# Optimization experiments

Hardware: AMD Instinct MI355X
Metric: run time of the kernel (lower is better)

## Reference

```python
import jax, jax.numpy as jnp
import numpy as np

B, S, HID = 2, 4096, 2048
H, D = 16, 128
BS = 64            # block_size
SR = 0.5           # sparsity_ratio
NB = S // BS       # number of diagonal blocks
SCALE = D ** -0.5


def setup_inputs() -> dict:
    key = jax.random.key(0)
    ks = jax.random.split(key, 7)
    s = 0.02
    return {
        "hidden_states": jax.random.normal(ks[0], (B, S, HID), jnp.float32),
        "Wq": jax.random.normal(ks[1], (HID, H * D), jnp.float32) * s,
        "Wk": jax.random.normal(ks[2], (HID, H * D), jnp.float32) * s,
        "Wv": jax.random.normal(ks[3], (HID, H * D), jnp.float32) * s,
        "Wo": jax.random.normal(ks[4], (H * D, HID), jnp.float32) * s,
        "Wr": jax.random.normal(ks[5], (HID, H), jnp.float32) * s,   # block_router weight
        "br": jax.random.normal(ks[6], (H,), jnp.float32) * s,       # block_router bias
    }


def reference(hidden_states, Wq, Wk, Wv, Wo, Wr, br):
    # projections: torch Linear(x) == x @ W^T; weights stored pre-transposed here
    q = (hidden_states @ Wq).reshape(B, S, H, D).transpose(0, 2, 1, 3)  # [B,H,S,D]
    k = (hidden_states @ Wk).reshape(B, S, H, D).transpose(0, 2, 1, 3)
    v = (hidden_states @ Wv).reshape(B, S, H, D).transpose(0, 2, 1, 3)

    # per-head routing score, mean-pooled over batch (as in torch: routing_scores[:, h].mean())
    routing = jax.nn.sigmoid(hidden_states.mean(axis=1) @ Wr + br)      # [B,H]
    head_score = routing.mean(axis=0)                                   # [H]
    eff_sparsity = SR * (1.0 - head_score * 0.5)
    # torch: max(1, int(block_size * eff)); positive -> floor == int truncation
    attend_count = jnp.maximum(1, jnp.floor(BS * eff_sparsity).astype(jnp.int32))  # [H]

    # block-diagonal attention: only within-block scores are ever finite, so we
    # never materialize the full SxS matrix (softmax over -inf elsewhere is a no-op)
    qb = q.reshape(B, H, NB, BS, D)
    kb = k.reshape(B, H, NB, BS, D)
    vb = v.reshape(B, H, NB, BS, D)
    scores = jnp.einsum("bhnqd,bhnkd->bhnqk", qb, kb) * SCALE           # [B,H,NB,BS,BS]

    # rank of each key within its row (descending); keep == variable-k top-k mask.
    order = jnp.argsort(-scores, axis=-1)
    rank = jnp.argsort(order, axis=-1)
    keep = rank < attend_count[None, :, None, None, None]
    # non-top-k in-block entries are scattered as 0.0 (not -inf) in the original
    masked = jnp.where(keep, scores, 0.0)

    probs = jax.nn.softmax(masked.astype(jnp.float32), axis=-1).astype(q.dtype)
    out_b = jnp.einsum("bhnqk,bhnkd->bhnqd", probs, vb)                 # [B,H,NB,BS,D]
    out = out_b.reshape(B, H, S, D).transpose(0, 2, 1, 3).reshape(B, S, H * D)
    return out @ Wo
```

## Files before the change

kernel.cpp:

```cpp
#include <hip/hip_runtime.h>
#include <hip/hip_bf16.h>
#include <cstdint>
#include <cstddef>

#define B_   2
#define S_   4096
#define HIDN 2048
#define H_   16
#define D_   128
#define NB_  64
#define MTOT 8192
#define QKVN 6144
#define SCALE_ 0.08838834764831845f

typedef unsigned short ushort_t;
typedef __attribute__((ext_vector_type(8))) short short8;
typedef __attribute__((ext_vector_type(8))) ushort_t ushort8;
typedef __attribute__((ext_vector_type(4))) float f32x4;

__device__ inline float b2f(ushort_t x){ union{unsigned u; float f;} v; v.u=((unsigned)x)<<16; return v.f; }
__device__ inline ushort_t f2b(float f){ union{unsigned u; float f;} v; v.f=f; unsigned r=(v.u + 0x7FFF + ((v.u>>16)&1))>>16; return (ushort_t)r; }

#define MFMA_BF16(a,b,c) __builtin_amdgcn_mfma_f32_16x16x32_bf16((a),(b),(c),0,0,0)

__device__ inline void async16(const ushort_t* g, ushort_t* l){
  __builtin_amdgcn_global_load_lds(
      (const __attribute__((address_space(1))) void*)g,
      (__attribute__((address_space(3))) void*)l, 16, 0, 0);
}

__global__ void bsa_convpart(const float* __restrict__ hs, ushort_t* __restrict__ hsB,
                             float* __restrict__ part){
  int t = threadIdx.x;
  int c  = blockIdx.x*512 + t*2;
  int sc = blockIdx.y;
  int b  = blockIdx.z;
  const float* p = hs  + ((size_t)b*S_ + (size_t)sc*128)*HIDN + c;
  ushort_t*    q = hsB + ((size_t)b*S_ + (size_t)sc*128)*HIDN + c;
  float s0=0.f, s1=0.f;
  #pragma unroll 8
  for (int i=0;i<128;i++){
    float2 v = *(const float2*)(p + (size_t)i*HIDN);
    s0 += v.x; s1 += v.y;
    unsigned pk = (unsigned)f2b(v.x) | ((unsigned)f2b(v.y)<<16);
    *(unsigned*)(q + (size_t)i*HIDN) = pk;
  }
  part[((b*32+sc)*HIDN)+c]   = s0;
  part[((b*32+sc)*HIDN)+c+1] = s1;
}

__global__ void bsa_router(const float* __restrict__ part, const float* __restrict__ Wr,
                           const float* __restrict__ br, int* __restrict__ counts){
  __shared__ float cm[2*HIDN];
  __shared__ float sig[2*H_];
  int t = threadIdx.x;
  for (int i=t; i<2*HIDN; i+=256){
    int b = i>>11, c = i&(HIDN-1);
    float s=0.f;
    for (int j=0;j<32;j++) s += part[((b*32+j)*HIDN)+c];
    cm[b*HIDN+c] = s * (1.0f/S_);
  }
  __syncthreads();
  {
    int g = t>>3;
    int sl = t&7;
    int b = g>>4, h = g&15;
    float acc = 0.f;
    for (int c=sl; c<HIDN; c+=8) acc += cm[b*HIDN+c]*Wr[c*H_+h];
    acc += __shfl_xor(acc, 4);
    acc += __shfl_xor(acc, 2);
    acc += __shfl_xor(acc, 1);
    if (sl==0) sig[g] = 1.f/(1.f+expf(-(acc + br[h])));
  }
  __syncthreads();
  if (t < H_){
    float score = 0.5f*(sig[t] + sig[H_+t]);
    float eff = 0.5f*(1.0f - score*0.5f);
    int ac = (int)floorf(64.f*eff);
    if (ac < 1) ac = 1;
    counts[t] = ac;
  }
}

__global__ void bsa_transpose(const float* w0, const float* w1, const float* w2, const float* w3,
                              ushort_t* o0, ushort_t* o1, ushort_t* o2, ushort_t* o3){
  const float* src; ushort_t* dst;
  switch(blockIdx.z){
    case 0: src=w0; dst=o0; break;
    case 1: src=w1; dst=o1; break;
    case 2: src=w2; dst=o2; break;
    default: src=w3; dst=o3; break;
  }
  __shared__ ushort_t tile[64*72];
  int t = threadIdx.x;
  int r0 = blockIdx.y*64, c0 = blockIdx.x*64;
  for (int it=0; it<16; it++){
    int f = it*256 + t;
    int r = f>>6, c = f&63;
    tile[r*72+c] = f2b(src[(size_t)(r0+r)*HIDN + (c0+c)]);
  }
  __syncthreads();
  for (int it=0; it<16; it++){
    int f = it*256 + t;
    int cc = f>>6, rr = f&63;
    dst[(size_t)(c0+cc)*HIDN + (r0+rr)] = tile[rr*72+cc];
  }
}

template<int F32OUT, int MINW>
__global__ __launch_bounds__(256, MINW) void bsa_gemm_bt(const ushort_t* __restrict__ A,
                                                   const ushort_t* __restrict__ BT,
                                                   void* __restrict__ Cv,
                                                   int M, int N, int K){
  __shared__ __align__(16) ushort_t As[128*32];
  __shared__ __align__(16) ushort_t Bs[128*32];
  int t = threadIdx.x;
  int w = t>>6, lane = t&63;
  int wr = w>>1, wc = w&1;
  int quad = lane>>4, l16 = lane&15;
  int m0 = blockIdx.y*128, n0 = blockIdx.x*128;

  f32x4 acc[4][4] = {};

  int srow = (w*2)*16 + (lane>>2);
  int scol = (lane&3)*8;

  for (int k0=0; k0<K; k0+=32){
    #pragma unroll
    for (int i=0;i<2;i++){
      int chunk = w*2+i;
      const ushort_t* ga = A  + (size_t)(m0 + srow + i*16)*K + k0 + scol;
      const ushort_t* gb = BT + (size_t)(n0 + srow + i*16)*K + k0 + scol;
      async16(ga, &As[chunk*512]);
      async16(gb, &Bs[chunk*512]);
    }
    __syncthreads();
    short8 a[4], b[4];
    #pragma unroll
    for (int i=0;i<4;i++)
      a[i] = *(const short8*)(&As[(wr*64 + i*16 + l16)*32 + quad*8]);
    #pragma unroll
    for (int j=0;j<4;j++)
      b[j] = *(const short8*)(&Bs[(wc*64 + j*16 + l16)*32 + quad*8]);
    #pragma unroll
    for (int i=0;i<4;i++)
      #pragma unroll
      for (int j=0;j<4;j++)
        acc[i][j] = MFMA_BF16(a[i], b[j], acc[i][j]);
    __syncthreads();
  }

  #pragma unroll
  for (int i=0;i<4;i++)
    #pragma unroll
    for (int j=0;j<4;j++){
      int m = m0 + wr*64 + i*16 + quad*4;
      int n = n0 + wc*64 + j*16 + l16;
      #pragma unroll
      for (int r=0;r<4;r++){
        if (F32OUT) ((float*)Cv)[(size_t)(m+r)*N + n] = acc[i][j][r];
        else        ((ushort_t*)Cv)[(size_t)(m+r)*N + n] = f2b(acc[i][j][r]);
      }
    }
}

__global__ __launch_bounds__(256) void bsa_attn(const ushort_t* __restrict__ QKV,
                                                const int* __restrict__ counts,
                                                ushort_t* __restrict__ O){
  __shared__ __align__(16) ushort_t regA[64*136];
  __shared__ __align__(16) ushort_t regB[64*136];
  __shared__ __align__(16) ushort_t Ps[64*72];
  float* Sc = (float*)regA;

  int t = threadIdx.x, w = t>>6, lane = t&63, quad = lane>>4, l16 = lane&15;
  int bid = blockIdx.x;
  int b  = bid>>10;
  int h  = (bid>>6)&15;
  int nb = bid&63;
  size_t qbase = ((size_t)b*S_ + (size_t)nb*64)*QKVN + (size_t)h*D_;
  size_t obase = ((size_t)b*S_ + (size_t)nb*64)*HIDN + (size_t)h*D_;

  int4 vre[4];
  #pragma unroll
  for (int it=0; it<4; it++){
    int f = it*256 + t;
    int r = f>>4, c = (f&15)*8;
    vre[it] = *(const int4*)(QKV + qbase + 4096 + (size_t)r*QKVN + c);
  }

  #pragma unroll
  for (int it=0; it<4; it++){
    int f = it*256 + t;
    int r = f>>4, c = (f&15)*8;
    *(int4*)(&regA[r*136+c]) = *(const int4*)(QKV + qbase +        (size_t)r*QKVN + c);
    *(int4*)(&regB[r*136+c]) = *(const int4*)(QKV + qbase + 2048 + (size_t)r*QKVN + c);
  }
  __syncthreads();

  f32x4 sacc[4] = {};
  #pragma unroll
  for (int ks=0; ks<4; ks++){
    short8 afr = *(const short8*)(&regA[(w*16 + l16)*136 + ks*32 + quad*8]);
    #pragma unroll
    for (int nt=0; nt<4; nt++){
      short8 bfr = *(const short8*)(&regB[(nt*16 + l16)*136 + ks*32 + quad*8]);
      sacc[nt] = MFMA_BF16(afr, bfr, sacc[nt]);
    }
  }
  __syncthreads();

  #pragma unroll
  for (int nt=0; nt<4; nt++)
    #pragma unroll
    for (int r=0;r<4;r++)
      Sc[(w*16 + quad*4 + r)*68 + nt*16 + l16] = sacc[nt][r]*SCALE_;
  #pragma unroll
  for (int it=0; it<4; it++){
    int f = it*256 + t;
    int r = f>>4, c = (f&15)*8;
    *(int4*)(&regB[r*136+c]) = vre[it];
  }

  int cnt = counts[h];
  for (int g=0; g<4; g++){
    float s[4], v[4];
    #pragma unroll
    for (int rr=0; rr<4; rr++){
      s[rr] = Sc[(w*16 + g*4 + rr)*68 + lane];
      v[rr] = s[rr];
    }
    #pragma unroll
    for (int k=2; k<=64; k<<=1){
      #pragma unroll
      for (int m=k>>1; m>=1; m>>=1){
        #pragma unroll
        for (int rr=0; rr<4; rr++){
          float o = __shfl_xor(v[rr], m);
          bool keepMin = (((lane & k)==0) == ((lane & m)==0));
          float lo = fminf(v[rr], o), hi = fmaxf(v[rr], o);
          v[rr] = keepMin ? lo : hi;
        }
      }
    }
    #pragma unroll
    for (int rr=0; rr<4; rr++){
      float T = __shfl(v[rr], 64 - cnt);
      unsigned long long gt = __ballot(s[rr] > T);
      unsigned long long eq = __ballot(s[rr] == T);
      int G = __popcll(gt);
      int eqr = __popcll(eq & ((1ull<<lane)-1ull));
      bool keep = (s[rr] > T) || ((s[rr] == T) && (eqr < cnt - G));
      float m = keep ? s[rr] : 0.0f;
      float mx = fmaxf(__shfl(v[rr], 63), 0.0f);
      float e = __expf(m - mx);
      float sum = e;
      #pragma unroll
      for (int off=32; off; off>>=1) sum += __shfl_xor(sum, off);
      Ps[(w*16 + g*4 + rr)*72 + lane] = f2b(e/sum);
    }
  }
  __syncthreads();

  f32x4 oacc[4][2] = {};
  #pragma unroll
  for (int ks=0; ks<2; ks++){
    short8 bv[2];
    #pragma unroll
    for (int jj=0; jj<2; jj++){
      int n = (w*2+jj)*16 + l16;
      short8 x;
      #pragma unroll
      for (int j=0;j<8;j++){
        int k = ks*32 + quad*8 + j;
        x[j] = (short)regB[k*136 + n];
      }
      bv[jj] = x;
    }
    #pragma unroll
    for (int mt=0; mt<4; mt++){
      short8 aP = *(const short8*)(&Ps[(mt*16 + l16)*72 + ks*32 + quad*8]);
      #pragma unroll
      for (int jj=0; jj<2; jj++)
        oacc[mt][jj] = MFMA_BF16(aP, bv[jj], oacc[mt][jj]);
    }
  }
  #pragma unroll
  for (int mt=0; mt<4; mt++)
    #pragma unroll
    for (int jj=0; jj<2; jj++){
      int row = mt*16 + quad*4;
      int col = (w*2+jj)*16 + l16;
      #pragma unroll
      for (int r=0;r<4;r++)
        O[obase + (size_t)(row+r)*HIDN + col] = f2b(oacc[mt][jj][r]);
    }
}

extern "C" void kernel_launch(void* const* d_in, const int* in_sizes, int n_in,
                              void* d_out, int out_size, void* d_ws, size_t ws_size,
                              hipStream_t stream) {
  const float* hs = (const float*)d_in[0];
  const float* Wq = (const float*)d_in[1];
  const float* Wk = (const float*)d_in[2];
  const float* Wv = (const float*)d_in[3];
  const float* Wo = (const float*)d_in[4];
  const float* Wr = (const float*)d_in[5];
  const float* br = (const float*)d_in[6];
  float* out = (float*)d_out;
  char* ws = (char*)d_ws;

  const size_t MB = 1024u*1024u;
  float*    part   = (float*)(ws + 0);
  int*      counts = (int*)(ws + 512u*1024u);
  ushort_t* hsB    = (ushort_t*)(ws + 1*MB);
  ushort_t* WqT    = (ushort_t*)(ws + 33*MB);
  ushort_t* WkT    = (ushort_t*)(ws + 41*MB);
  ushort_t* WvT    = (ushort_t*)(ws + 49*MB);
  ushort_t* WoT    = (ushort_t*)(ws + 57*MB);
  ushort_t* QKV    = (ushort_t*)(ws + 65*MB);
  ushort_t* AO     = hsB;

  bsa_convpart  <<<dim3(4,32,2),  256, 0, stream>>>(hs, hsB, part);
  bsa_router    <<<1,             256, 0, stream>>>(part, Wr, br, counts);
  bsa_transpose <<<dim3(32,32,4), 256, 0, stream>>>(Wq,Wk,Wv,Wo, WqT,WkT,WvT,WoT);
  bsa_gemm_bt<0,4><<<dim3(48,64), 256, 0, stream>>>(hsB, WqT, (void*)QKV, MTOT, QKVN, 2048);
  bsa_attn      <<<2048,          256, 0, stream>>>(QKV, counts, AO);
  bsa_gemm_bt<1,4><<<dim3(16,64), 256, 0, stream>>>(AO, WoT, (void*)out, MTOT, 2048, 2048);
}
```

Baseline: 712.2 us.

## Replace GEMM with 256x256 double-buffered swizzled-LDS pipelined MFMA kernel

```diff
diff --git a/kernel.cpp b/kernel.cpp
--- a/kernel.cpp
+++ b/kernel.cpp
@@ -107,59 +107,135 @@
   }
 }
 
-template<int F32OUT, int MINW>
-__global__ __launch_bounds__(256, MINW) void bsa_gemm_bt(const ushort_t* __restrict__ A,
-                                                   const ushort_t* __restrict__ BT,
-                                                   void* __restrict__ Cv,
-                                                   int M, int N, int K){
-  __shared__ __align__(16) ushort_t As[128*32];
-  __shared__ __align__(16) ushort_t Bs[128*32];
+
+#define SBAR asm volatile("s_barrier" ::: "memory")
+#define WLGK asm volatile("s_waitcnt lgkmcnt(0)" ::: "memory")
+#define WVM4 asm volatile("s_waitcnt vmcnt(4)" ::: "memory")
+#define WVM0 asm volatile("s_waitcnt vmcnt(0)" ::: "memory")
+#define PHI  __builtin_amdgcn_s_setprio(1)
+#define PLO  __builtin_amdgcn_s_setprio(0)
+
+__device__ __forceinline__ short8 lds_frag(const ushort_t* buf, int row, int kb){
+  int off = ((row<<7) + kb) ^ ((row&7)<<4);
+  return *(const short8*)((const char*)buf + off);
+}
+
+__device__ __forceinline__ void rd_a(short8 (&a)[4][2], const ushort_t* buf, int r0, int l16, int quad){
+  #pragma unroll
+  for (int mi=0; mi<4; mi++)
+    #pragma unroll
+    for (int ks=0; ks<2; ks++)
+      a[mi][ks] = lds_frag(buf, r0 + mi*16 + l16, ks*64 + quad*16);
+}
+__device__ __forceinline__ void rd_b(short8 (&b)[2][2], const ushort_t* buf, int r0, int l16, int quad){
+  #pragma unroll
+  for (int ni=0; ni<2; ni++)
+    #pragma unroll
+    for (int ks=0; ks<2; ks++)
+      b[ni][ks] = lds_frag(buf, r0 + ni*16 + l16, ks*64 + quad*16);
+}
+__device__ __forceinline__ void mm8(f32x4 (&acc)[8][4], const short8 (&a)[4][2],
+                                    const short8 (&b)[2][2], int mo, int no){
+  #pragma unroll
+  for (int mi=0; mi<4; mi++)
+    #pragma unroll
+    for (int ni=0; ni<2; ni++){
+      acc[mo+mi][no+ni] = MFMA_BF16(a[mi][0], b[ni][0], acc[mo+mi][no+ni]);
+      acc[mo+mi][no+ni] = MFMA_BF16(a[mi][1], b[ni][1], acc[mo+mi][no+ni]);
+    }
+}
+__device__ __forceinline__ void stage_half(ushort_t* ldsHalf, const ushort_t* g,
+                                           int K, int w, int roff, int coff){
+  async16(g + (size_t)(w*16 + roff)*K + coff,     ldsHalf + (w*2+0)*512);
+  async16(g + (size_t)(w*16 + 8 + roff)*K + coff, ldsHalf + (w*2+1)*512);
+}
+
+template<int F32OUT>
+__global__ __launch_bounds__(512, 2) void bsa_gemm8(const ushort_t* __restrict__ A,
+                                                    const ushort_t* __restrict__ BT,
+                                                    void* __restrict__ Cv,
+                                                    int M, int N, int K){
+  extern __shared__ __align__(16) ushort_t sm[];
+  ushort_t* A0  = sm;
+  ushort_t* A1  = sm + 16384;
+  ushort_t* Bb0 = sm + 32768;
+  ushort_t* Bb1 = sm + 49152;
+
   int t = threadIdx.x;
-  int w = t>>6, lane = t&63;
-  int wr = w>>1, wc = w&1;
-  int quad = lane>>4, l16 = lane&15;
-  int m0 = blockIdx.y*128, n0 = blockIdx.x*128;
-
-  f32x4 acc[4][4] = {};
-
-  int srow = (w*2)*16 + (lane>>2);
-  int scol = (lane&3)*8;
-
-  for (int k0=0; k0<K; k0+=32){
-    #pragma unroll
-    for (int i=0;i<2;i++){
-      int chunk = w*2+i;
-      const ushort_t* ga = A  + (size_t)(m0 + srow + i*16)*K + k0 + scol;
-      const ushort_t* gb = BT + (size_t)(n0 + srow + i*16)*K + k0 + scol;
-      async16(ga, &As[chunk*512]);
-      async16(gb, &Bs[chunk*512]);
-    }
-    __syncthreads();
-    short8 a[4], b[4];
-    #pragma unroll
-    for (int i=0;i<4;i++)
-      a[i] = *(const short8*)(&As[(wr*64 + i*16 + l16)*32 + quad*8]);
-    #pragma unroll
-    for (int j=0;j<4;j++)
-      b[j] = *(const short8*)(&Bs[(wc*64 + j*16 + l16)*32 + quad*8]);
-    #pragma unroll
-    for (int i=0;i<4;i++)
-      #pragma unroll
-      for (int j=0;j<4;j++)
-        acc[i][j] = MFMA_BF16(a[i], b[j], acc[i][j]);
-    __syncthreads();
-  }
-
-  #pragma unroll
-  for (int i=0;i<4;i++)
-    #pragma unroll
-    for (int j=0;j<4;j++){
-      int m = m0 + wr*64 + i*16 + quad*4;
-      int n = n0 + wc*64 + j*16 + l16;
+  int w = t>>6, lane = t&63, quad = lane>>4, l16 = lane&15;
+  int wr = w>>2, wc = w&3;
+
+  int nbx = N>>8;
+  int nwg = (M>>8)*nbx;
+  int bid = blockIdx.x;
+  int swz = (bid&7)*(nwg>>3) + (bid>>3);
+  int bx = swz % nbx, by = swz / nbx;
+  int m0 = by<<8, n0 = bx<<8;
+
+  const ushort_t* Ag = A  + (size_t)m0*K;
+  const ushort_t* Bg = BT + (size_t)n0*K;
+  int roff = lane>>3;
+  int coff = ((lane&7) ^ roff) << 3;
+
+  f32x4 acc[8][4] = {};
+  short8 a[4][2], b0[2][2], b1[2][2];
+
+  stage_half(A0,        Ag,                      K, w, roff, coff);
+  stage_half(A0+8192,   Ag + (size_t)128*K,      K, w, roff, coff);
+  stage_half(Bb0,       Bg,                      K, w, roff, coff);
+  stage_half(Bb0+8192,  Bg + (size_t)128*K,      K, w, roff, coff);
+  stage_half(Bb1,       Bg + 64,                 K, w, roff, coff);
+  stage_half(Bb1+8192,  Bg + (size_t)128*K + 64, K, w, roff, coff);
+  WVM4;
+  SBAR;
+
+  int nit = K>>7;
+  #pragma unroll 1
+  for (int i=0; i<nit; i++){
+    bool notlast = (i+1 < nit);
+    int kA  = (2*i+1)*64;
+    int kN0 = (2*i+2)*64;
+    int kN1 = (2*i+3)*64;
+    rd_a(a, A0, wr*128, l16, quad);
+    rd_b(b0, Bb0, wc*64, l16, quad);
+    stage_half(A1, Ag + kA, K, w, roff, coff);
+    SBAR; WLGK; PHI; mm8(acc, a, b0, 0,0); PLO; SBAR;
+    rd_b(b1, Bb0, wc*64+32, l16, quad);
+    stage_half(A1+8192, Ag + (size_t)128*K + kA, K, w, roff, coff);
+    SBAR; WLGK; PHI; mm8(acc, a, b1, 0,2); PLO; SBAR;
+    rd_a(a, A0, wr*128+64, l16, quad);
+    if (notlast) stage_half(Bb0, Bg + kN0, K, w, roff, coff);
+    SBAR; WLGK; PHI; mm8(acc, a, b0, 4,0); PLO; SBAR;
+    if (notlast) stage_half(Bb0+8192, Bg + (size_t)128*K + kN0, K, w, roff, coff);
+    SBAR; PHI; mm8(acc, a, b1, 4,2); PLO;
+    if (notlast) { WVM4; } else { WVM0; }
+    SBAR;
+    rd_a(a, A1, wr*128, l16, quad);
+    rd_b(b0, Bb1, wc*64, l16, quad);
+    if (notlast) stage_half(A0, Ag + kN0, K, w, roff, coff);
+    SBAR; WLGK; PHI; mm8(acc, a, b0, 0,0); PLO; SBAR;
+    rd_b(b1, Bb1, wc*64+32, l16, quad);
+    if (notlast) stage_half(A0+8192, Ag + (size_t)128*K + kN0, K, w, roff, coff);
+    SBAR; WLGK; PHI; mm8(acc, a, b1, 0,2); PLO; SBAR;
+    rd_a(a, A1, wr*128+64, l16, quad);
+    if (notlast) stage_half(Bb1, Bg + kN1, K, w, roff, coff);
+    SBAR; WLGK; PHI; mm8(acc, a, b0, 4,0); PLO; SBAR;
+    if (notlast) stage_half(Bb1+8192, Bg + (size_t)128*K + kN1, K, w, roff, coff);
+    SBAR; PHI; mm8(acc, a, b1, 4,2); PLO;
+    if (notlast) { WVM4; } else { WVM0; }
+    SBAR;
+  }
+
+  #pragma unroll
+  for (int mi=0; mi<8; mi++)
+    #pragma unroll
+    for (int ni=0; ni<4; ni++){
+      int m = m0 + wr*128 + mi*16 + quad*4;
+      int n = n0 + wc*64 + ni*16 + l16;
       #pragma unroll
       for (int r=0;r<4;r++){
-        if (F32OUT) ((float*)Cv)[(size_t)(m+r)*N + n] = acc[i][j][r];
-        else        ((ushort_t*)Cv)[(size_t)(m+r)*N + n] = f2b(acc[i][j][r]);
+        if (F32OUT) ((float*)Cv)[(size_t)(m+r)*N + n] = acc[mi][ni][r];
+        else        ((ushort_t*)Cv)[(size_t)(m+r)*N + n] = f2b(acc[mi][ni][r]);
       }
     }
 }
@@ -320,10 +396,19 @@
   ushort_t* QKV    = (ushort_t*)(ws + 65*MB);
   ushort_t* AO     = hsB;
 
+  static bool attr_done = false;
+  if (!attr_done){
+    hipFuncSetAttribute((const void*)&bsa_gemm8<0>,
+                        hipFuncAttributeMaxDynamicSharedMemorySize, 131072);
+    hipFuncSetAttribute((const void*)&bsa_gemm8<1>,
+                        hipFuncAttributeMaxDynamicSharedMemorySize, 131072);
+    attr_done = true;
+  }
+
   bsa_convpart  <<<dim3(4,32,2),  256, 0, stream>>>(hs, hsB, part);
   bsa_router    <<<1,             256, 0, stream>>>(part, Wr, br, counts);
   bsa_transpose <<<dim3(32,32,4), 256, 0, stream>>>(Wq,Wk,Wv,Wo, WqT,WkT,WvT,WoT);
-  bsa_gemm_bt<0,4><<<dim3(48,64), 256, 0, stream>>>(hsB, WqT, (void*)QKV, MTOT, QKVN, 2048);
+  bsa_gemm8<0><<<dim3(768), 512, 131072, stream>>>(hsB, WqT, (void*)QKV, MTOT, QKVN, 2048);
   bsa_attn      <<<2048,          256, 0, stream>>>(QKV, counts, AO);
-  bsa_gemm_bt<1,4><<<dim3(16,64), 256, 0, stream>>>(AO, WoT, (void*)out, MTOT, 2048, 2048);
-}
+  bsa_gemm8<1><<<dim3(256), 512, 131072, stream>>>(AO, WoT, (void*)out, MTOT, 2048, 2048);
+}
```

Result: faster. 662.2 us (-7.0%).
